# Kernel optimization log

Hardware: AMD Instinct MI355X
Metric: run time of the kernel (lower is better)

## Reference

```python
import jax, jax.numpy as jnp
import numpy as np

N = 8192
E = 512
EPS = 1e-12  # F.normalize default eps


def setup_inputs() -> dict:
    key = jax.random.key(0)
    ks = jax.random.split(key, 7)
    scale = 1.0 / np.sqrt(E)  # roughly match nn.Linear init scale
    return {
        "x": jax.random.normal(ks[0], (N, E), dtype=jnp.float32),
        "Wq": jax.random.normal(ks[1], (E, E), dtype=jnp.float32) * scale,
        "bq": jax.random.normal(ks[2], (E,), dtype=jnp.float32) * scale,
        "Wk": jax.random.normal(ks[3], (E, E), dtype=jnp.float32) * scale,
        "bk": jax.random.normal(ks[4], (E,), dtype=jnp.float32) * scale,
        "Wv": jax.random.normal(ks[5], (E, E), dtype=jnp.float32) * scale,
        "bv": jax.random.normal(ks[6], (E,), dtype=jnp.float32) * scale,
    }


def reference(x, Wq, bq, Wk, bk, Wv, bv):
    # torch nn.Linear: y = x @ W^T + b
    q = x @ Wq.T + bq  # [N, E]
    k = x @ Wk.T + bk  # [N, E]
    v = x @ Wv.T + bv  # [N, E]
    s = q @ k.T  # [N, N]
    # F.normalize(s): L2-normalize each row (dim=1), norm clamped to eps
    norm = jnp.maximum(jnp.linalg.norm(s, axis=1, keepdims=True), EPS)
    w = s / norm
    # F.softmax default dim for 2-D input is dim=1
    w = jax.nn.softmax(w, axis=1)
    return w @ v  # [N, E]
```

## Files before the change

### kernel.cpp

```cpp
#include <hip/hip_runtime.h>
#include <hip/hip_bf16.h>

typedef unsigned short u16;
typedef unsigned int u32;
typedef short short8 __attribute__((ext_vector_type(8)));
typedef float fvec4 __attribute__((ext_vector_type(4)));

#define NR 8192
#define ED 512
#define PSTR 264

__device__ inline u16 f2bf(float f) {
    union { float f; unsigned u; } c; c.f = f;
    unsigned u = c.u;
    u += 0x7FFFu + ((u >> 16) & 1u);
    return (u16)(u >> 16);
}
__device__ inline float bf2f(u16 h) {
    union { unsigned u; float f; } c; c.u = ((unsigned)h) << 16; return c.f;
}
__device__ inline short8 load_cvt8(const float* p) {
    const fvec4* q = (const fvec4*)p;
    fvec4 a = q[0], b = q[1];
    short8 r;
    r[0] = (short)f2bf(a[0]); r[1] = (short)f2bf(a[1]);
    r[2] = (short)f2bf(a[2]); r[3] = (short)f2bf(a[3]);
    r[4] = (short)f2bf(b[0]); r[5] = (short)f2bf(b[1]);
    r[6] = (short)f2bf(b[2]); r[7] = (short)f2bf(b[3]);
    return r;
}
__device__ inline void gload16(const void* g, void* l) {
    __builtin_amdgcn_global_load_lds(
        (const __attribute__((address_space(1))) u32*)g,
        (__attribute__((address_space(3))) u32*)l, 16, 0, 0);
}

#define SWZ_SCOL(lane) ((((lane) & 7) ^ ((lane) >> 3)) * 8)
#define SWZ_RD(col, row) ((col) ^ (((row) & 7) * 8))

__global__ __launch_bounds__(256) void cvt_kernel(
    const float* __restrict__ x, const float* __restrict__ Wq,
    const float* __restrict__ Wk, const float* __restrict__ Wv,
    u16* __restrict__ xb, u16* __restrict__ wb)
{
    int tid = blockIdx.x * 256 + threadIdx.x;
    const float* src; u16* dst; int off;
    if (tid < 524288)      { src = x;  dst = xb;          off = tid; }
    else if (tid < 557056) { src = Wq; dst = wb;          off = tid - 524288; }
    else if (tid < 589824) { src = Wk; dst = wb + 262144; off = tid - 557056; }
    else                   { src = Wv; dst = wb + 524288; off = tid - 589824; }
    *(short8*)(dst + (size_t)off * 8) = load_cvt8(src + (size_t)off * 8);
}

__global__ __launch_bounds__(256, 3) void qkv_kernel(
    const u16* __restrict__ xb, const u16* __restrict__ wb,
    const float* __restrict__ bq, const float* __restrict__ bk, const float* __restrict__ bv,
    u16* __restrict__ qb, u16* __restrict__ kb, u16* __restrict__ kT, u16* __restrict__ vT)
{
    __shared__ u16 ldsA[128][64];
    __shared__ u16 ldsB[128][64];

    const int lane = threadIdx.x & 63;
    const int w = threadIdx.x >> 6;
    const int ln = lane & 15;
    const int kg = lane >> 4;
    const int wr = w >> 1, wc = w & 1;
    const int z = blockIdx.z;
    const int R0 = blockIdx.y * 128;
    const int C0 = blockIdx.x * 128;
    const int srow = lane >> 3;
    const int scol = SWZ_SCOL(lane);

    const u16* B = wb + (size_t)z * 262144;
    const float* bias = (z == 0) ? bq : (z == 1) ? bk : bv;

    fvec4 acc[4][4];
    #pragma unroll
    for (int m = 0; m < 4; ++m)
        #pragma unroll
        for (int n = 0; n < 4; ++n) acc[m][n] = (fvec4){0.f, 0.f, 0.f, 0.f};

    for (int kt = 0; kt < 8; ++kt) {
        const int k0 = kt * 64;
        __syncthreads();
        #pragma unroll
        for (int i = 0; i < 4; ++i) {
            const int ra = (i * 4 + w) * 8;
            gload16(xb + (size_t)(R0 + ra + srow) * ED + k0 + scol, &ldsA[ra][0]);
            gload16(B  + (size_t)(C0 + ra + srow) * ED + k0 + scol, &ldsB[ra][0]);
        }
        __syncthreads();
        short8 af[2][4], bf8[2][4];
        #pragma unroll
        for (int kk = 0; kk < 2; ++kk) {
            #pragma unroll
            for (int m = 0; m < 4; ++m) {
                const int row = wr * 64 + m * 16 + ln;
                af[kk][m] = *(const short8*)&ldsA[row][SWZ_RD(kk * 32 + kg * 8, row)];
            }
            #pragma unroll
            for (int n = 0; n < 4; ++n) {
                const int row = wc * 64 + n * 16 + ln;
                bf8[kk][n] = *(const short8*)&ldsB[row][SWZ_RD(kk * 32 + kg * 8, row)];
            }
        }
        #pragma unroll
        for (int kk = 0; kk < 2; ++kk)
            #pragma unroll
            for (int m = 0; m < 4; ++m)
                #pragma unroll
                for (int n = 0; n < 4; ++n)
                    acc[m][n] = __builtin_amdgcn_mfma_f32_16x16x32_bf16(af[kk][m], bf8[kk][n], acc[m][n], 0, 0, 0);
    }

    #pragma unroll
    for (int n = 0; n < 4; ++n) {
        const int gcol = C0 + wc * 64 + n * 16 + ln;
        const float bc = bias[gcol];
        #pragma unroll
        for (int m = 0; m < 4; ++m) {
            #pragma unroll
            for (int r = 0; r < 4; ++r) {
                const int grow = R0 + wr * 64 + m * 16 + kg * 4 + r;
                u16 val = f2bf(acc[m][n][r] + bc);
                if (z == 0) {
                    qb[(size_t)grow * ED + gcol] = val;
                } else if (z == 1) {
                    kb[(size_t)grow * ED + gcol] = val;
                    kT[(size_t)gcol * NR + grow] = val;
                } else {
                    vT[(size_t)gcol * NR + grow] = val;
                }
            }
        }
    }
}

__global__ __launch_bounds__(256) void gram_kernel(
    const u16* __restrict__ kT, u16* __restrict__ Gb)
{
    __shared__ float red[4][64][4];
    const int lane = threadIdx.x & 63;
    const int w = threadIdx.x >> 6;
    const int ln = lane & 15;
    const int kg = lane >> 4;
    const int i0 = (blockIdx.x >> 5) * 16, l0 = (blockIdx.x & 31) * 16;

    fvec4 acc[4];
    #pragma unroll
    for (int c = 0; c < 4; ++c) acc[c] = (fvec4){0.f, 0.f, 0.f, 0.f};
    const u16* arow = kT + (size_t)(i0 + ln) * NR + w * 2048 + kg * 8;
    const u16* brow = kT + (size_t)(l0 + ln) * NR + w * 2048 + kg * 8;
    #pragma unroll 8
    for (int t = 0; t < 64; ++t) {
        acc[t & 3] = __builtin_amdgcn_mfma_f32_16x16x32_bf16(
            *(const short8*)(arow + t * 32), *(const short8*)(brow + t * 32), acc[t & 3], 0, 0, 0);
    }
    fvec4 s = acc[0] + acc[1] + acc[2] + acc[3];
    #pragma unroll
    for (int r = 0; r < 4; ++r) red[w][lane][r] = s[r];
    __syncthreads();
    if (w == 0) {
        #pragma unroll
        for (int r = 0; r < 4; ++r) {
            float tot = red[0][lane][r] + red[1][lane][r] + red[2][lane][r] + red[3][lane][r];
            Gb[(size_t)(i0 + kg * 4 + r) * ED + l0 + ln] = f2bf(tot);
        }
    }
}

__global__ __launch_bounds__(256) void rn_kernel(
    const u16* __restrict__ qb, const u16* __restrict__ Gb, float* __restrict__ rn)
{
    __shared__ float red[4][16];
    const int lane = threadIdx.x & 63;
    const int wv = threadIdx.x >> 6;
    const int ln = lane & 15;
    const int kg = lane >> 4;
    const int m0 = blockIdx.x * 16;

    short8 afr[16];
    const u16* qrow = qb + (size_t)(m0 + ln) * ED + kg * 8;
    #pragma unroll
    for (int t = 0; t < 16; ++t) afr[t] = *(const short8*)(qrow + t * 32);

    float ss[4] = {0.f, 0.f, 0.f, 0.f};
    for (int ee = 0; ee < 8; ++ee) {
        const int e = wv * 8 + ee;
        fvec4 a0 = (fvec4){0.f, 0.f, 0.f, 0.f};
        fvec4 a1 = (fvec4){0.f, 0.f, 0.f, 0.f};
        const u16* grow = Gb + (size_t)(e * 16 + ln) * ED + kg * 8;
        #pragma unroll
        for (int t = 0; t < 16; t += 2) {
            a0 = __builtin_amdgcn_mfma_f32_16x16x32_bf16(afr[t],     *(const short8*)(grow + t * 32),       a0, 0, 0, 0);
            a1 = __builtin_amdgcn_mfma_f32_16x16x32_bf16(afr[t + 1], *(const short8*)(grow + (t + 1) * 32), a1, 0, 0, 0);
        }
        fvec4 acc = a0 + a1;
        #pragma unroll
        for (int r = 0; r < 4; ++r)
            ss[r] += acc[r] * bf2f(qb[(size_t)(m0 + kg * 4 + r) * ED + e * 16 + ln]);
    }
    #pragma unroll
    for (int r = 0; r < 4; ++r) {
        float v = ss[r];
        v += __shfl_xor(v, 1); v += __shfl_xor(v, 2);
        v += __shfl_xor(v, 4); v += __shfl_xor(v, 8);
        ss[r] = v;
    }
    if (ln == 0) {
        #pragma unroll
        for (int r = 0; r < 4; ++r) red[wv][kg * 4 + r] = ss[r];
    }
    __syncthreads();
    if (threadIdx.x < 16) {
        const int row = threadIdx.x;
        const float tot = red[0][row] + red[1][row] + red[2][row] + red[3][row];
        rn[m0 + row] = 1.0f / fmaxf(sqrtf(tot), 1e-12f);
    }
}

__global__ __launch_bounds__(256, 3) void sexp_kernel(
    const u16* __restrict__ qb, const u16* __restrict__ kb,
    const float* __restrict__ rn, u16* __restrict__ P, float* __restrict__ dsum)
{
    __shared__ u16 ldsA[128][64];
    __shared__ u16 ldsB[128][64];

    const int lane = threadIdx.x & 63;
    const int w = threadIdx.x >> 6;
    const int ln = lane & 15;
    const int kg = lane >> 4;
    const int wr = w >> 1, wc = w & 1;
    const int R0 = blockIdx.y * 128;
    const int C0 = blockIdx.x * 128;
    const int srow = lane >> 3;
    const int scol = SWZ_SCOL(lane);

    fvec4 acc[4][4];
    #pragma unroll
    for (int m = 0; m < 4; ++m)
        #pragma unroll
        for (int n = 0; n < 4; ++n) acc[m][n] = (fvec4){0.f, 0.f, 0.f, 0.f};

    for (int kt = 0; kt < 8; ++kt) {
        const int k0 = kt * 64;
        __syncthreads();
        #pragma unroll
        for (int i = 0; i < 4; ++i) {
            const int ra = (i * 4 + w) * 8;
            gload16(qb + (size_t)(R0 + ra + srow) * ED + k0 + scol, &ldsA[ra][0]);
            gload16(kb + (size_t)(C0 + ra + srow) * ED + k0 + scol, &ldsB[ra][0]);
        }
        __syncthreads();
        short8 af[2][4], bf8[2][4];
        #pragma unroll
        for (int kk = 0; kk < 2; ++kk) {
            #pragma unroll
            for (int m = 0; m < 4; ++m) {
                const int row = wr * 64 + m * 16 + ln;
                af[kk][m] = *(const short8*)&ldsA[row][SWZ_RD(kk * 32 + kg * 8, row)];
            }
            #pragma unroll
            for (int n = 0; n < 4; ++n) {
                const int row = wc * 64 + n * 16 + ln;
                bf8[kk][n] = *(const short8*)&ldsB[row][SWZ_RD(kk * 32 + kg * 8, row)];
            }
        }
        #pragma unroll
        for (int kk = 0; kk < 2; ++kk)
            #pragma unroll
            for (int m = 0; m < 4; ++m)
                #pragma unroll
                for (int n = 0; n < 4; ++n)
                    acc[m][n] = __builtin_amdgcn_mfma_f32_16x16x32_bf16(af[kk][m], bf8[kk][n], acc[m][n], 0, 0, 0);
    }

    #pragma unroll
    for (int m = 0; m < 4; ++m) {
        float dpart[4] = {0.f, 0.f, 0.f, 0.f};
        #pragma unroll
        for (int r = 0; r < 4; ++r) {
            const int grow = R0 + wr * 64 + m * 16 + kg * 4 + r;
            const float rv = rn[grow];
            #pragma unroll
            for (int n = 0; n < 4; ++n) {
                const int gcol = C0 + wc * 64 + n * 16 + ln;
                u16 pb = f2bf(__expf(acc[m][n][r] * rv));
                P[(size_t)grow * NR + gcol] = pb;
                dpart[r] += bf2f(pb);
            }
        }
        #pragma unroll
        for (int r = 0; r < 4; ++r) {
            float v = dpart[r];
            v += __shfl_xor(v, 1); v += __shfl_xor(v, 2);
            v += __shfl_xor(v, 4); v += __shfl_xor(v, 8);
            if (ln == 0)
                atomicAdd(&dsum[R0 + wr * 64 + m * 16 + kg * 4 + r], v);
        }
    }
}

__global__ __launch_bounds__(256, 4) void pv_kernel(
    const u16* __restrict__ P, const u16* __restrict__ vT, float* __restrict__ part,
    int ksteps)
{
    __shared__ u16 ldsA[128][64];
    __shared__ u16 ldsB[128][64];

    const int lane = threadIdx.x & 63;
    const int w = threadIdx.x >> 6;
    const int ln = lane & 15;
    const int kg = lane >> 4;
    const int wr = w >> 1, wc = w & 1;
    const int id2 = blockIdx.y * gridDim.x + blockIdx.x;
    const int tile = ((id2 & 7) << 5) + (id2 >> 3);
    const int R0 = (tile >> 2) * 128;
    const int C0 = (tile & 3) * 128;
    const int ks = blockIdx.z;
    const int srow = lane >> 3;
    const int scol = SWZ_SCOL(lane);

    float* pp = part + (size_t)ks * NR * ED;

    fvec4 acc[4][4];
    #pragma unroll
    for (int m = 0; m < 4; ++m)
        #pragma unroll
        for (int n = 0; n < 4; ++n) acc[m][n] = (fvec4){0.f, 0.f, 0.f, 0.f};

    for (int kt = 0; kt < ksteps; ++kt) {
        const int k0 = (ks * ksteps + kt) * 64;
        __syncthreads();
        #pragma unroll
        for (int i = 0; i < 4; ++i) {
            const int ra = (i * 4 + w) * 8;
            gload16(P  + (size_t)(R0 + ra + srow) * NR + k0 + scol, &ldsA[ra][0]);
            gload16(vT + (size_t)(C0 + ra + srow) * NR + k0 + scol, &ldsB[ra][0]);
        }
        __syncthreads();
        short8 af[2][4], bf8[2][4];
        #pragma unroll
        for (int kk = 0; kk < 2; ++kk) {
            #pragma unroll
            for (int m = 0; m < 4; ++m) {
                const int row = wr * 64 + m * 16 + ln;
                af[kk][m] = *(const short8*)&ldsA[row][SWZ_RD(kk * 32 + kg * 8, row)];
            }
            #pragma unroll
            for (int n = 0; n < 4; ++n) {
                const int row = wc * 64 + n * 16 + ln;
                bf8[kk][n] = *(const short8*)&ldsB[row][SWZ_RD(kk * 32 + kg * 8, row)];
            }
        }
        #pragma unroll
        for (int kk = 0; kk < 2; ++kk)
            #pragma unroll
            for (int m = 0; m < 4; ++m)
                #pragma unroll
                for (int n = 0; n < 4; ++n)
                    acc[m][n] = __builtin_amdgcn_mfma_f32_16x16x32_bf16(af[kk][m], bf8[kk][n], acc[m][n], 0, 0, 0);
    }

    #pragma unroll
    for (int m = 0; m < 4; ++m) {
        #pragma unroll
        for (int r = 0; r < 4; ++r) {
            const int grow = R0 + wr * 64 + m * 16 + kg * 4 + r;
            #pragma unroll
            for (int n = 0; n < 4; ++n) {
                const int gcol = C0 + wc * 64 + n * 16 + ln;
                pp[(size_t)grow * ED + gcol] = acc[m][n][r];
            }
        }
    }
}

__global__ __launch_bounds__(256) void reduce_kernel(
    const float* __restrict__ part, const float* __restrict__ dsum,
    float* __restrict__ out, int nsplit)
{
    const size_t idx = ((size_t)blockIdx.x * 256 + threadIdx.x) * 4;
    const int row = (int)(idx >> 9);
    const float iv = 1.0f / dsum[row];
    fvec4 s = *(const fvec4*)(part + idx);
    for (int k = 1; k < nsplit; ++k) {
        fvec4 b = *(const fvec4*)(part + (size_t)k * NR * ED + idx);
        #pragma unroll
        for (int i = 0; i < 4; ++i) s[i] += b[i];
    }
    fvec4 o;
    #pragma unroll
    for (int i = 0; i < 4; ++i) o[i] = s[i] * iv;
    *(fvec4*)(out + idx) = o;
}

__global__ __launch_bounds__(512, 2) void attn_kernel(
    const u16* __restrict__ qb, const u16* __restrict__ kb,
    const u16* __restrict__ vT, const float* __restrict__ rn, float* __restrict__ out)
{
    __shared__ u16 p_lds[2 * 16 * PSTR];
    __shared__ float red[2][4][16];

    const int lane = threadIdx.x & 63;
    const int w = threadIdx.x >> 6;
    const int ln = lane & 15;
    const int kg = lane >> 4;
    const int rh = w >> 2;
    const int jg = w & 3;
    const int R0 = blockIdx.x * 32 + rh * 16;

    short8 afr[16];
    const u16* qrow = qb + (size_t)(R0 + ln) * ED + kg * 8;
    #pragma unroll
    for (int t = 0; t < 16; ++t) afr[t] = *(const short8*)(qrow + t * 32);

    float rnv[4];
    #pragma unroll
    for (int r = 0; r < 4; ++r) rnv[r] = rn[R0 + kg * 4 + r];

    fvec4 oacc[8];
    #pragma unroll
    for (int e = 0; e < 8; ++e) oacc[e] = (fvec4){0.f, 0.f, 0.f, 0.f};
    float dsum[4] = {0.f, 0.f, 0.f, 0.f};

    u16* pw = p_lds + rh * 16 * PSTR;

    for (int c = 0; c < 32; ++c) {
        const int j0 = c * 256 + jg * 64;
        fvec4 acc[4];
        #pragma unroll
        for (int jt = 0; jt < 4; ++jt) acc[jt] = (fvec4){0.f, 0.f, 0.f, 0.f};
        const u16* kbase = kb + (size_t)(j0 + ln) * ED + kg * 8;
        #pragma unroll 4
        for (int t = 0; t < 16; ++t) {
            short8 af = afr[t];
            #pragma unroll
            for (int jt = 0; jt < 4; ++jt) {
                short8 bfr = *(const short8*)(kbase + (size_t)jt * 16 * ED + t * 32);
                acc[jt] = __builtin_amdgcn_mfma_f32_16x16x32_bf16(af, bfr, acc[jt], 0, 0, 0);
            }
        }
        #pragma unroll
        for (int jt = 0; jt < 4; ++jt) {
            #pragma unroll
            for (int r = 0; r < 4; ++r) {
                float p = __expf(acc[jt][r] * rnv[r]);
                dsum[r] += p;
                pw[(kg * 4 + r) * PSTR + jg * 64 + jt * 16 + ln] = f2bf(p);
            }
        }
        __syncthreads();
        const u16* vbase = vT + (size_t)(jg * 128 + ln) * NR + c * 256 + kg * 8;
        const u16* prow = pw + ln * PSTR + kg * 8;
        #pragma unroll
        for (int kk = 0; kk < 8; ++kk) {
            short8 afp = *(const short8*)(prow + kk * 32);
            #pragma unroll
            for (int e = 0; e < 8; ++e) {
                short8 bfr = *(const short8*)(vbase + (size_t)e * 16 * NR + kk * 32);
                oacc[e] = __builtin_amdgcn_mfma_f32_16x16x32_bf16(afp, bfr, oacc[e], 0, 0, 0);
            }
        }
        __syncthreads();
    }

    #pragma unroll
    for (int r = 0; r < 4; ++r) {
        float v = dsum[r];
        v += __shfl_xor(v, 1); v += __shfl_xor(v, 2);
        v += __shfl_xor(v, 4); v += __shfl_xor(v, 8);
        dsum[r] = v;
    }
    if (ln == 0) {
        #pragma unroll
        for (int r = 0; r < 4; ++r) red[rh][jg][kg * 4 + r] = dsum[r];
    }
    __syncthreads();
    float inv[4];
    #pragma unroll
    for (int r = 0; r < 4; ++r) {
        const int row = kg * 4 + r;
        inv[r] = 1.0f / (red[rh][0][row] + red[rh][1][row] + red[rh][2][row] + red[rh][3][row]);
    }
    #pragma unroll
    for (int e = 0; e < 8; ++e) {
        #pragma unroll
        for (int r = 0; r < 4; ++r)
            out[(size_t)(R0 + kg * 4 + r) * ED + jg * 128 + e * 16 + ln] = oacc[e][r] * inv[r];
    }
}

extern "C" void kernel_launch(void* const* d_in, const int* in_sizes, int n_in,
                              void* d_out, int out_size, void* d_ws, size_t ws_size,
                              hipStream_t stream) {
    const float* x  = (const float*)d_in[0];
    const float* Wq = (const float*)d_in[1];
    const float* bq = (const float*)d_in[2];
    const float* Wk = (const float*)d_in[3];
    const float* bk = (const float*)d_in[4];
    const float* Wv = (const float*)d_in[5];
    const float* bv = (const float*)d_in[6];
    float* out = (float*)d_out;

    u16* xb = (u16*)d_ws;
    u16* wb = xb + (size_t)NR * ED;
    u16* qb = wb + 3 * 262144;
    u16* kb = qb + (size_t)NR * ED;
    u16* kT = kb + (size_t)NR * ED;
    u16* vT = kT + (size_t)NR * ED;
    u16* Gb = vT + (size_t)NR * ED;
    float* rn   = (float*)(Gb + 262144);
    float* dsum = rn + NR;
    u16* P = (u16*)(dsum + NR);

    const size_t need = (size_t)((u16*)(dsum + NR) - (u16*)d_ws) * 2 + (size_t)NR * NR * 2;
    const size_t need4 = need + (size_t)4 * NR * ED * sizeof(float);

    cvt_kernel<<<2432, 256, 0, stream>>>(x, Wq, Wk, Wv, xb, wb);
    dim3 g1(ED / 128, NR / 128, 3);
    qkv_kernel<<<g1, 256, 0, stream>>>(xb, wb, bq, bk, bv, qb, kb, kT, vT);
    gram_kernel<<<1024, 256, 0, stream>>>(kT, Gb);
    rn_kernel<<<512, 256, 0, stream>>>(qb, Gb, rn);

    if (ws_size >= need) {
        hipMemsetAsync(dsum, 0, NR * sizeof(float), stream);
        dim3 gs(NR / 128, NR / 128);
        sexp_kernel<<<gs, 256, 0, stream>>>(qb, kb, rn, P, dsum);

        int nsplit; float* part;
        if (ws_size >= need4) {
            nsplit = 4;
            part = (float*)(P + (size_t)NR * NR);
        } else {
            nsplit = 2;
            part = (float*)d_ws;
        }
        dim3 gp(ED / 128, NR / 128, nsplit);
        pv_kernel<<<gp, 256, 0, stream>>>(P, vT, part, 128 / nsplit);
        reduce_kernel<<<NR * ED / 4 / 256, 256, 0, stream>>>(part, dsum, out, nsplit);
    } else {
        attn_kernel<<<NR / 32, 512, 0, stream>>>(qb, kb, vT, rn, out);
    }
}
```

Measured before the change: 334.4 us.

## Move K/V transposes to an LDS transpose kernel and double-buffer PV loads

The QKV projection now writes row-major Q, K and V only. A new LDS-tiled transpose kernel builds K^T and V^T with coalesced 16-byte stores, replacing the strided scattered stores in the projection epilogue. The PV GEMM gets double-buffered LDS so the next tile's global loads overlap the current tile's MFMAs, and its occupancy hint drops from 4 to 2. The sexp kernel's occupancy hint rises from 3 to 4. This adds an extra kernel launch and an extra round trip of K/V through memory, and doubles the PV kernel's LDS use.

Result: slower. 398.3 us (+19.1%).

```diff
diff --git a/kernel.cpp b/kernel.cpp
--- a/kernel.cpp
+++ b/kernel.cpp
@@ -55,7 +55,7 @@
 __global__ __launch_bounds__(256, 3) void qkv_kernel(
     const u16* __restrict__ xb, const u16* __restrict__ wb,
     const float* __restrict__ bq, const float* __restrict__ bk, const float* __restrict__ bv,
-    u16* __restrict__ qb, u16* __restrict__ kb, u16* __restrict__ kT, u16* __restrict__ vT)
+    u16* __restrict__ qb, u16* __restrict__ kb, u16* __restrict__ vb)
 {
     __shared__ u16 ldsA[128][64];
     __shared__ u16 ldsB[128][64];
@@ -73,6 +73,7 @@
 
     const u16* B = wb + (size_t)z * 262144;
     const float* bias = (z == 0) ? bq : (z == 1) ? bk : bv;
+    u16* dst = (z == 0) ? qb : (z == 1) ? kb : vb;
 
     fvec4 acc[4][4];
     #pragma unroll
@@ -122,18 +123,39 @@
             #pragma unroll
             for (int r = 0; r < 4; ++r) {
                 const int grow = R0 + wr * 64 + m * 16 + kg * 4 + r;
-                u16 val = f2bf(acc[m][n][r] + bc);
-                if (z == 0) {
-                    qb[(size_t)grow * ED + gcol] = val;
-                } else if (z == 1) {
-                    kb[(size_t)grow * ED + gcol] = val;
-                    kT[(size_t)gcol * NR + grow] = val;
-                } else {
-                    vT[(size_t)gcol * NR + grow] = val;
-                }
-            }
-        }
-    }
+                dst[(size_t)grow * ED + gcol] = f2bf(acc[m][n][r] + bc);
+            }
+        }
+    }
+}
+
+__global__ __launch_bounds__(256) void tr_kernel(
+    const u16* __restrict__ kb, const u16* __restrict__ vb,
+    u16* __restrict__ kT, u16* __restrict__ vT)
+{
+    __shared__ u16 tile[64][65];
+    const int z = blockIdx.z;
+    const u16* src = z ? vb : kb;
+    u16* dst = z ? vT : kT;
+    const int R0 = blockIdx.y * 64;
+    const int C0 = blockIdx.x * 64;
+    const int t = threadIdx.x;
+    const int r = t >> 2;
+    const int c0 = (t & 3) * 16;
+
+    const u16* s = src + (size_t)(R0 + r) * ED + C0 + c0;
+    *(short8*)&tile[r][c0]     = *(const short8*)s;
+    *(short8*)&tile[r][c0 + 8] = *(const short8*)(s + 8);
+    __syncthreads();
+
+    const int cc = t >> 2;
+    const int r0 = (t & 3) * 16;
+    u16 tmp[16];
+    #pragma unroll
+    for (int j = 0; j < 16; ++j) tmp[j] = tile[r0 + j][cc];
+    u16* d = dst + (size_t)(C0 + cc) * NR + R0 + r0;
+    *(short8*)d       = *(short8*)&tmp[0];
+    *(short8*)(d + 8) = *(short8*)&tmp[8];
 }
 
 __global__ __launch_bounds__(256) void gram_kernel(
@@ -219,7 +241,7 @@
     }
 }
 
-__global__ __launch_bounds__(256, 3) void sexp_kernel(
+__global__ __launch_bounds__(256, 4) void sexp_kernel(
     const u16* __restrict__ qb, const u16* __restrict__ kb,
     const float* __restrict__ rn, u16* __restrict__ P, float* __restrict__ dsum)
 {
@@ -301,12 +323,12 @@
     }
 }
 
-__global__ __launch_bounds__(256, 4) void pv_kernel(
+__global__ __launch_bounds__(256, 2) void pv_kernel(
     const u16* __restrict__ P, const u16* __restrict__ vT, float* __restrict__ part,
     int ksteps)
 {
-    __shared__ u16 ldsA[128][64];
-    __shared__ u16 ldsB[128][64];
+    __shared__ u16 ldsA[2][128][64];
+    __shared__ u16 ldsB[2][128][64];
 
     const int lane = threadIdx.x & 63;
     const int w = threadIdx.x >> 6;
@@ -329,28 +351,38 @@
         #pragma unroll
         for (int n = 0; n < 4; ++n) acc[m][n] = (fvec4){0.f, 0.f, 0.f, 0.f};
 
+    const int kbase = ks * ksteps * 64;
+    #pragma unroll
+    for (int i = 0; i < 4; ++i) {
+        const int ra = (i * 4 + w) * 8;
+        gload16(P  + (size_t)(R0 + ra + srow) * NR + kbase + scol, &ldsA[0][ra][0]);
+        gload16(vT + (size_t)(C0 + ra + srow) * NR + kbase + scol, &ldsB[0][ra][0]);
+    }
+    __syncthreads();
+
+    int cur = 0;
     for (int kt = 0; kt < ksteps; ++kt) {
-        const int k0 = (ks * ksteps + kt) * 64;
-        __syncthreads();
-        #pragma unroll
-        for (int i = 0; i < 4; ++i) {
-            const int ra = (i * 4 + w) * 8;
-            gload16(P  + (size_t)(R0 + ra + srow) * NR + k0 + scol, &ldsA[ra][0]);
-            gload16(vT + (size_t)(C0 + ra + srow) * NR + k0 + scol, &ldsB[ra][0]);
-        }
-        __syncthreads();
+        if (kt + 1 < ksteps) {
+            const int k0n = kbase + (kt + 1) * 64;
+            #pragma unroll
+            for (int i = 0; i < 4; ++i) {
+                const int ra = (i * 4 + w) * 8;
+                gload16(P  + (size_t)(R0 + ra + srow) * NR + k0n + scol, &ldsA[cur ^ 1][ra][0]);
+                gload16(vT + (size_t)(C0 + ra + srow) * NR + k0n + scol, &ldsB[cur ^ 1][ra][0]);
+            }
+        }
         short8 af[2][4], bf8[2][4];
         #pragma unroll
         for (int kk = 0; kk < 2; ++kk) {
             #pragma unroll
             for (int m = 0; m < 4; ++m) {
                 const int row = wr * 64 + m * 16 + ln;
-                af[kk][m] = *(const short8*)&ldsA[row][SWZ_RD(kk * 32 + kg * 8, row)];
+                af[kk][m] = *(const short8*)&ldsA[cur][row][SWZ_RD(kk * 32 + kg * 8, row)];
             }
             #pragma unroll
             for (int n = 0; n < 4; ++n) {
                 const int row = wc * 64 + n * 16 + ln;
-                bf8[kk][n] = *(const short8*)&ldsB[row][SWZ_RD(kk * 32 + kg * 8, row)];
+                bf8[kk][n] = *(const short8*)&ldsB[cur][row][SWZ_RD(kk * 32 + kg * 8, row)];
             }
         }
         #pragma unroll
@@ -360,6 +392,8 @@
                 #pragma unroll
                 for (int n = 0; n < 4; ++n)
                     acc[m][n] = __builtin_amdgcn_mfma_f32_16x16x32_bf16(af[kk][m], bf8[kk][n], acc[m][n], 0, 0, 0);
+        __syncthreads();
+        cur ^= 1;
     }
 
     #pragma unroll
@@ -507,19 +541,23 @@
     u16* wb = xb + (size_t)NR * ED;
     u16* qb = wb + 3 * 262144;
     u16* kb = qb + (size_t)NR * ED;
-    u16* kT = kb + (size_t)NR * ED;
+    u16* vb = kb + (size_t)NR * ED;
+    u16* kT = vb + (size_t)NR * ED;
     u16* vT = kT + (size_t)NR * ED;
     u16* Gb = vT + (size_t)NR * ED;
     float* rn   = (float*)(Gb + 262144);
     float* dsum = rn + NR;
     u16* P = (u16*)(dsum + NR);
 
-    const size_t need = (size_t)((u16*)(dsum + NR) - (u16*)d_ws) * 2 + (size_t)NR * NR * 2;
+    const size_t base  = (size_t)((char*)(dsum + NR) - (char*)d_ws);
+    const size_t need  = base + (size_t)NR * NR * 2;
     const size_t need4 = need + (size_t)4 * NR * ED * sizeof(float);
 
     cvt_kernel<<<2432, 256, 0, stream>>>(x, Wq, Wk, Wv, xb, wb);
     dim3 g1(ED / 128, NR / 128, 3);
-    qkv_kernel<<<g1, 256, 0, stream>>>(xb, wb, bq, bk, bv, qb, kb, kT, vT);
+    qkv_kernel<<<g1, 256, 0, stream>>>(xb, wb, bq, bk, bv, qb, kb, vb);
+    dim3 gt(ED / 64, NR / 64, 2);
+    tr_kernel<<<gt, 256, 0, stream>>>(kb, vb, kT, vT);
     gram_kernel<<<1024, 256, 0, stream>>>(kT, Gb);
     rn_kernel<<<512, 256, 0, stream>>>(qb, Gb, rn);
 
```
